# Kernel tuning notes

Hardware: AMD Instinct MI355X
Metric: run time of the kernel (lower is better)

## Reference

```python
import jax, jax.numpy as jnp
import numpy as np

B = 2048      # number of sequences with non-empty history
S = 32        # seq_len (all sequences full length for static shapes)
H = 256       # h_dim == embd_rank (ent/rel embedding dim)
NSEG = B * S  # total history timesteps (segments)
NNBR = 524288 # total gathered neighbor embeddings (avg 8 per segment)
ENT = 100000
REL = 1000


def setup_inputs() -> dict:
    key = jax.random.key(0)
    k1, k2, k3, k4, k5, k6, k7 = jax.random.split(key, 7)
    return {
        "neighbor_idx": jax.random.randint(k1, (NNBR,), 0, ENT),
        "segment_ids": jnp.sort(jax.random.randint(k2, (NNBR,), 0, NSEG)),
        "s_tem": jax.random.randint(k3, (B,), 0, ENT),
        "r_tem": jax.random.randint(k4, (B,), 0, REL),
        "s_hist_dt": jax.random.uniform(k5, (NSEG,), dtype=jnp.float32),
        "ent_embeds": jax.random.normal(k6, (ENT, H), dtype=jnp.float32),
        "rel_embeds": jax.random.normal(k7, (REL, H), dtype=jnp.float32),
    }


def reference(neighbor_idx, segment_ids, s_tem, r_tem, s_hist_dt, ent_embeds, rel_embeds):
    # gather neighbor entity embeddings (embeds_stack in the original)
    embeds_stack = ent_embeds[neighbor_idx]                     # [NNBR, H]
    # sparse.mm(mask, embeds_stack) == segment sum over neighbor groups
    sums = jax.ops.segment_sum(embeds_stack, segment_ids, num_segments=NSEG)
    counts = jax.ops.segment_sum(jnp.ones((NNBR,), embeds_stack.dtype),
                                 segment_ids, num_segments=NSEG)
    embeds_mean = sums / jnp.maximum(counts, 1.0)[:, None]      # [NSEG, H]
    # scatter means into padded [B, S, H] (all sequences full length)
    mean_seq = embeds_mean.reshape(B, S, H)
    # repeat subject entity / relation embeddings along time and concat
    ent_b = jnp.broadcast_to(ent_embeds[s_tem][:, None, :], (B, S, H))
    rel_b = jnp.broadcast_to(rel_embeds[r_tem][:, None, :], (B, S, H))
    s_embed_seq = jnp.concatenate([mean_seq, ent_b, rel_b], axis=-1)  # [B, S, 3H]
    s_hist_dt_seq = s_hist_dt.reshape(B, S)
    return s_embed_seq, s_hist_dt_seq
```

## Files before the change

kernel.cpp:

```cpp
#include <hip/hip_runtime.h>
#include <hip/hip_bf16.h>

#define BB    2048
#define SS    32
#define HH    256
#define NSEGC 65536
#define NNBRC 524288
#define NXCD  8

using f32x4 = __attribute__((ext_vector_type(4))) float;

__global__ __launch_bounds__(256) void seg_bounds_dt_kernel(
    const int*   __restrict__ segment_ids,
    int*         __restrict__ start,
    const float* __restrict__ dt,
    float*       __restrict__ out_tail)
{
    const int i = blockIdx.x * blockDim.x + threadIdx.x;

    if (i < NSEGC / 4) {
        const f32x4 v = reinterpret_cast<const f32x4*>(dt)[i];
        __builtin_nontemporal_store(v, reinterpret_cast<f32x4*>(out_tail) + i);
    }

    if (i > NSEGC) return;
    int lo = 0, hi = NNBRC;
    while (lo < hi) {
        const int mid = (lo + hi) >> 1;
        if (segment_ids[mid] < i) lo = mid + 1;
        else hi = mid;
    }
    start[i] = lo;
}

__global__ __launch_bounds__(256) void agg_kernel(
    const int*   __restrict__ neighbor_idx,
    const int*   __restrict__ s_tem,
    const int*   __restrict__ r_tem,
    const float* __restrict__ ent,
    const float* __restrict__ rel,
    const int*   __restrict__ start,
    float*       __restrict__ out)
{
    const int chunk = gridDim.x / NXCD;
    const int wg    = (blockIdx.x % NXCD) * chunk + blockIdx.x / NXCD;

    const int seg  = wg * 4 + (threadIdx.x >> 6);
    const int lane = threadIdx.x & 63;
    if (seg >= NSEGC) return;
    const int b = seg >> 5;

    const int begin = start[seg];
    const int end   = start[seg + 1];

    float ax = 0.f, ay = 0.f, az = 0.f, aw = 0.f;

    for (int base = begin; base < end; base += 64) {
        const int cnt = min(64, end - base);
        int myidx = 0;
        if (lane < cnt) myidx = neighbor_idx[base + lane];
        #pragma unroll 4
        for (int j = 0; j < cnt; ++j) {
            const int nbr = __shfl(myidx, j);
            const f32x4 v = *reinterpret_cast<const f32x4*>(
                ent + (size_t)nbr * HH + lane * 4);
            ax += v.x; ay += v.y; az += v.z; aw += v.w;
        }
    }

    const float inv = 1.0f / fmaxf((float)(end - begin), 1.0f);
    f32x4 m;
    m.x = ax * inv; m.y = ay * inv; m.z = az * inv; m.w = aw * inv;

    float* o = out + (size_t)seg * (3 * HH);
    __builtin_nontemporal_store(m, reinterpret_cast<f32x4*>(o) + lane);

    const int e = s_tem[b];
    const f32x4 ev = *reinterpret_cast<const f32x4*>(
        ent + (size_t)e * HH + lane * 4);
    __builtin_nontemporal_store(ev, reinterpret_cast<f32x4*>(o + HH) + lane);

    const int r = r_tem[b];
    const f32x4 rv = *reinterpret_cast<const f32x4*>(
        rel + (size_t)r * HH + lane * 4);
    __builtin_nontemporal_store(rv, reinterpret_cast<f32x4*>(o + 2 * HH) + lane);
}

extern "C" void kernel_launch(void* const* d_in, const int* in_sizes, int n_in,
                              void* d_out, int out_size, void* d_ws, size_t ws_size,
                              hipStream_t stream) {
    const int*   neighbor_idx = (const int*)  d_in[0];
    const int*   segment_ids  = (const int*)  d_in[1];
    const int*   s_tem        = (const int*)  d_in[2];
    const int*   r_tem        = (const int*)  d_in[3];
    const float* s_hist_dt    = (const float*)d_in[4];
    const float* ent_embeds   = (const float*)d_in[5];
    const float* rel_embeds   = (const float*)d_in[6];
    float*       out          = (float*)d_out;

    int* start = (int*)d_ws;

    {
        const int threads = 256;
        const int total   = NSEGC + 1;
        const int blocks  = (total + threads - 1) / threads;
        float* out_tail = out + (size_t)NSEGC * (3 * HH);
        seg_bounds_dt_kernel<<<blocks, threads, 0, stream>>>(
            segment_ids, start, s_hist_dt, out_tail);
    }

    {
        const int threads = 256;
        const int blocks  = NSEGC / 4;
        agg_kernel<<<blocks, threads, 0, stream>>>(
            neighbor_idx, s_tem, r_tem, ent_embeds, rel_embeds, start, out);
    }
}
```

Baseline: 338.8 us.

## Process four segments per wave with batched 8-wide gathers

Each wavefront now handles four consecutive segments instead of one. It walks their combined neighbor range and issues up to eight independent row gathers before accumulating each into the matching segment's accumulator. The s_tem/r_tem rows are loaded once and stored for all four segments. The goal is more memory-level parallelism per wave and less per-segment overhead for short segments. The cost is fewer waves in flight (grid is four times smaller), more registers, and branchy per-element segment selection.

```diff
diff --git a/kernel.cpp b/kernel.cpp
--- a/kernel.cpp
+++ b/kernel.cpp
@@ -7,6 +7,7 @@
 #define NSEGC 65536
 #define NNBRC 524288
 #define NXCD  8
+#define SPW   4
 
 using f32x4 = __attribute__((ext_vector_type(4))) float;
 
@@ -42,48 +43,78 @@
     const int*   __restrict__ start,
     float*       __restrict__ out)
 {
-    const int chunk = gridDim.x / NXCD;
-    const int wg    = (blockIdx.x % NXCD) * chunk + blockIdx.x / NXCD;
+    const int chunkw = gridDim.x / NXCD;
+    const int wg   = (blockIdx.x % NXCD) * chunkw + blockIdx.x / NXCD;
+    const int wave = wg * 4 + (threadIdx.x >> 6);
+    const int lane = threadIdx.x & 63;
+    const int seg0 = wave * SPW;
+    const int b    = seg0 >> 5;
 
-    const int seg  = wg * 4 + (threadIdx.x >> 6);
-    const int lane = threadIdx.x & 63;
-    if (seg >= NSEGC) return;
-    const int b = seg >> 5;
+    const int sv = start[seg0 + min(lane, SPW)];
+    const int p0 = __builtin_amdgcn_readfirstlane(__shfl(sv, 0));
+    const int p1 = __builtin_amdgcn_readfirstlane(__shfl(sv, 1));
+    const int p2 = __builtin_amdgcn_readfirstlane(__shfl(sv, 2));
+    const int p3 = __builtin_amdgcn_readfirstlane(__shfl(sv, 3));
+    const int p4 = __builtin_amdgcn_readfirstlane(__shfl(sv, 4));
+    const int total = p4 - p0;
+    const int r1 = p1 - p0, r2 = p2 - p0, r3 = p3 - p0;
 
-    const int begin = start[seg];
-    const int end   = start[seg + 1];
+    const int e = s_tem[b];
+    const int r = r_tem[b];
+    const f32x4 ev = *reinterpret_cast<const f32x4*>(ent + (size_t)e * HH + lane * 4);
+    const f32x4 rv = *reinterpret_cast<const f32x4*>(rel + (size_t)r * HH + lane * 4);
 
-    float ax = 0.f, ay = 0.f, az = 0.f, aw = 0.f;
+    f32x4 a0 = {0.f,0.f,0.f,0.f}, a1 = a0, a2 = a0, a3 = a0;
 
-    for (int base = begin; base < end; base += 64) {
-        const int cnt = min(64, end - base);
+    for (int base = 0; base < total; base += 64) {
+        const int cnt = min(64, total - base);
         int myidx = 0;
-        if (lane < cnt) myidx = neighbor_idx[base + lane];
-        #pragma unroll 4
-        for (int j = 0; j < cnt; ++j) {
-            const int nbr = __shfl(myidx, j);
-            const f32x4 v = *reinterpret_cast<const f32x4*>(
-                ent + (size_t)nbr * HH + lane * 4);
-            ax += v.x; ay += v.y; az += v.z; aw += v.w;
+        if (lane < cnt) myidx = neighbor_idx[p0 + base + lane];
+
+        for (int j = 0; j < cnt; j += 8) {
+            const int m = min(8, cnt - j);
+
+#define GLD(K, VK)                                                         \
+            f32x4 VK = {0.f,0.f,0.f,0.f};                                  \
+            if (K < m) {                                                   \
+                const int nb = __shfl(myidx, j + K);                       \
+                VK = *reinterpret_cast<const f32x4*>(                      \
+                    ent + (size_t)nb * HH + lane * 4);                     \
+            }
+            GLD(0, v0) GLD(1, v1) GLD(2, v2) GLD(3, v3)
+            GLD(4, v4) GLD(5, v5) GLD(6, v6) GLD(7, v7)
+#undef GLD
+
+#define ACC(K, VK)                                                         \
+            if (K < m) {                                                   \
+                const int p = base + j + K;                                \
+                if      (p < r1) a0 += VK;                                 \
+                else if (p < r2) a1 += VK;                                 \
+                else if (p < r3) a2 += VK;                                 \
+                else             a3 += VK;                                 \
+            }
+            ACC(0, v0) ACC(1, v1) ACC(2, v2) ACC(3, v3)
+            ACC(4, v4) ACC(5, v5) ACC(6, v6) ACC(7, v7)
+#undef ACC
         }
     }
 
-    const float inv = 1.0f / fmaxf((float)(end - begin), 1.0f);
-    f32x4 m;
-    m.x = ax * inv; m.y = ay * inv; m.z = az * inv; m.w = aw * inv;
+    const float i0 = 1.0f / fmaxf((float)(p1 - p0), 1.0f);
+    const float i1 = 1.0f / fmaxf((float)(p2 - p1), 1.0f);
+    const float i2 = 1.0f / fmaxf((float)(p3 - p2), 1.0f);
+    const float i3 = 1.0f / fmaxf((float)(p4 - p3), 1.0f);
 
-    float* o = out + (size_t)seg * (3 * HH);
-    __builtin_nontemporal_store(m, reinterpret_cast<f32x4*>(o) + lane);
-
-    const int e = s_tem[b];
-    const f32x4 ev = *reinterpret_cast<const f32x4*>(
-        ent + (size_t)e * HH + lane * 4);
-    __builtin_nontemporal_store(ev, reinterpret_cast<f32x4*>(o + HH) + lane);
-
-    const int r = r_tem[b];
-    const f32x4 rv = *reinterpret_cast<const f32x4*>(
-        rel + (size_t)r * HH + lane * 4);
-    __builtin_nontemporal_store(rv, reinterpret_cast<f32x4*>(o + 2 * HH) + lane);
+    float* o = out + (size_t)seg0 * (3 * HH);
+#define STROW(S, AV, INV)                                                  \
+    {                                                                      \
+        const f32x4 mm = AV * INV;                                         \
+        float* os = o + (size_t)(S) * (3 * HH);                            \
+        __builtin_nontemporal_store(mm, reinterpret_cast<f32x4*>(os) + lane);          \
+        __builtin_nontemporal_store(ev, reinterpret_cast<f32x4*>(os + HH) + lane);     \
+        __builtin_nontemporal_store(rv, reinterpret_cast<f32x4*>(os + 2 * HH) + lane); \
+    }
+    STROW(0, a0, i0) STROW(1, a1, i1) STROW(2, a2, i2) STROW(3, a3, i3)
+#undef STROW
 }
 
 extern "C" void kernel_launch(void* const* d_in, const int* in_sizes, int n_in,
@@ -102,8 +133,7 @@
 
     {
         const int threads = 256;
-        const int total   = NSEGC + 1;
-        const int blocks  = (total + threads - 1) / threads;
+        const int blocks  = (NSEGC + 1 + threads - 1) / threads;
         float* out_tail = out + (size_t)NSEGC * (3 * HH);
         seg_bounds_dt_kernel<<<blocks, threads, 0, stream>>>(
             segment_ids, start, s_hist_dt, out_tail);
@@ -111,7 +141,7 @@
 
     {
         const int threads = 256;
-        const int blocks  = NSEGC / 4;
+        const int blocks  = NSEGC / SPW / 4;
         agg_kernel<<<blocks, threads, 0, stream>>>(
             neighbor_idx, s_tem, r_tem, ent_embeds, rel_embeds, start, out);
     }
```

Result: no change. 336.6 us (-0.6%).
